# Kernel tuning notes

Measured on AMD Instinct MI355X. Metric: run time of the kernel, lower is better.

## Reference

```python
import jax, jax.numpy as jnp
import numpy as np
import math

B, CK, CV, H, W = 16, 64, 512, 56, 56


def setup_inputs() -> dict:
    key = jax.random.key(0)
    k1, k2, k3, k4 = jax.random.split(key, 4)
    return {
        "mk": jax.random.normal(k1, (B, CK, H, W), dtype=jnp.float32),
        "qk": jax.random.normal(k2, (B, CK, H, W), dtype=jnp.float32),
        "mv": jax.random.normal(k3, (B, CV, H, W), dtype=jnp.float32),
        "qv": jax.random.normal(k4, (B, CV, H, W), dtype=jnp.float32),
    }


def reference(mk, qk, mv, qv):
    b, ck, h, w = qk.shape
    cv = mv.shape[1]
    n = h * w
    qk_f = qk.reshape(b, ck, n)          # [B, CK, HW] query keys
    mk_f = mk.reshape(b, ck, -1)         # [B, CK, N_mem]
    # squared-L2 affinity (query-norm term is constant per column -> dropped, cancels in softmax)
    a = jnp.sum(mk_f * mk_f, axis=1)[:, :, None]                # [B, N_mem, 1]
    bb = 2.0 * jnp.einsum('bcn,bcm->bnm', mk_f, qk_f)           # [B, N_mem, HW]
    affinity = (-a + bb) / math.sqrt(ck)
    affinity = jax.nn.softmax(affinity, axis=1)                 # softmax over memory dim
    # readout: weighted sum of memory values
    mem = jnp.einsum('bcn,bnm->bcm', mv.reshape(b, cv, -1), affinity)
    mem = mem.reshape(b, cv, h, w)
    return mem, qv
```

## Files before the change

### kernel.cpp

```cpp
#include <hip/hip_runtime.h>


#define B_   16
#define CK_  64
#define CV_  512
#define N_   3136
#define NPAD 3200
#define TM   128
#define TN   128
#define NITER 25
#define NBLK32 100
#define NBLK16 200

typedef __bf16 bf16_t;
typedef bf16_t bf16x8 __attribute__((ext_vector_type(8)));
typedef bf16_t bf16x4 __attribute__((ext_vector_type(4)));
typedef float  f32x16 __attribute__((ext_vector_type(16)));
typedef float  f32x4  __attribute__((ext_vector_type(4)));

#define SCALE_DOT 0.36067376022224085f

__global__ __launch_bounds__(256) void prep_kq(const float* __restrict__ mk,
                                               const float* __restrict__ qk,
                                               bf16_t* __restrict__ Kf,
                                               bf16_t* __restrict__ Qf,
                                               float* __restrict__ a2) {
  int idx = blockIdx.x * 256 + threadIdx.x;
  int b = idx / NPAD, n = idx % NPAD;
  bool valid = n < N_;
  int l32n = n & 31, nblk = n >> 5;
  float ss = 0.f;
  const float* mkp = mk + (size_t)b * CK_ * N_ + n;
  const float* qkp = qk + (size_t)b * CK_ * N_ + n;
  bf16x8* Kf8 = (bf16x8*)Kf;
  bf16x8* Qf8 = (bf16x8*)Qf;
  #pragma unroll
  for (int cc = 0; cc < 8; cc++) {
    bf16x8 kv, qv8;
    #pragma unroll
    for (int j = 0; j < 8; j++) {
      int c = 8 * cc + j;
      float kx = valid ? mkp[(size_t)c * N_] : 0.f;
      float qx = valid ? qkp[(size_t)c * N_] : 0.f;
      ss += kx * kx;
      kv[j] = (bf16_t)kx;
      qv8[j] = (bf16_t)qx;
    }
    int s = cc >> 1, hh = cc & 1;
    size_t pos = (((size_t)b * NBLK32 + nblk) * 4 + s) * 64 + l32n + 32 * hh;
    Kf8[pos] = kv;
    Qf8[pos] = qv8;
  }
  a2[idx] = valid ? ss * 0.5f : 3.0e38f;
}

#define VCHUNK 512
__global__ __launch_bounds__(256) void prep_v(const float* __restrict__ mv,
                                              bf16_t* __restrict__ Vf) {
  __shared__ __align__(16) bf16_t T[32][VCHUNK];
  int wg = blockIdx.x;
  int chunk = wg % 7;
  int t2 = wg / 7;
  int cblk = t2 & 15;
  int b = t2 >> 4;
  int n0 = chunk * VCHUNK;
  int tid = threadIdx.x;

  const float* base = mv + ((size_t)b * CV_ + cblk * 32) * N_;
  #pragma unroll
  for (int rep = 0; rep < 16; rep++) {
    int idx = rep * 256 + tid;
    int cl = idx >> 7;
    int np = (idx & 127) * 4;
    int n = n0 + np;
    bf16x4 o;
    if (n < N_) {
      f32x4 v = *(const f32x4*)(base + (size_t)cl * N_ + n);
      #pragma unroll
      for (int j = 0; j < 4; j++) o[j] = (bf16_t)v[j];
    } else {
      #pragma unroll
      for (int j = 0; j < 4; j++) o[j] = (bf16_t)0.f;
    }
    *(bf16x4*)((char*)T + cl * (VCHUNK * 2) + ((np * 2) ^ ((cl & 7) << 4))) = o;
  }
  __syncthreads();

  bf16x8* Vf8 = (bf16x8*)Vf;
  size_t outbase = (((size_t)b * 16 + cblk) * NBLK16 + (n0 >> 4)) * 64;
  #pragma unroll
  for (int pass = 0; pass < 8; pass++) {
    int idx = pass * 256 + tid;
    int nb = idx >> 6;
    int ln = idx & 63;
    if (n0 + nb * 16 < NPAD) {
      int cl = ln & 31;
      int n_loc = nb * 16 + (ln >> 5) * 8;
      bf16x8 o = *(bf16x8*)((char*)T + cl * (VCHUNK * 2) +
                            ((n_loc * 2) ^ ((cl & 7) << 4)));
      Vf8[outbase + (size_t)nb * 64 + ln] = o;
    }
  }
}

__global__ __launch_bounds__(512, 2) void attn_main(const bf16_t* __restrict__ Kf,
                                                    const bf16_t* __restrict__ Qf,
                                                    const float* __restrict__ A2S,
                                                    const bf16_t* __restrict__ Vf,
                                                    const float* __restrict__ qv,
                                                    float* __restrict__ out) {
  const int xcd = blockIdx.x & 7;
  const int idx = blockIdx.x >> 3;
  const int q25 = idx / 25;
  const int b   = xcd * 2 + q25;
  const int m0  = (idx - q25 * 25) * TM;

  const int tid  = threadIdx.x;
  const int w    = tid >> 6;
  const int lane = tid & 63;
  const int l32  = lane & 31;
  const int h    = lane >> 5;
  const int g    = w >> 2;
  const int i    = w & 3;

  __shared__ __align__(16) char pool[65536];

  const bf16x8* Qf8 = (const bf16x8*)Qf;
  bf16x8 qfrag[2][4];
  #pragma unroll
  for (int jj = 0; jj < 2; jj++)
    #pragma unroll
    for (int s = 0; s < 4; s++)
      qfrag[jj][s] = Qf8[(((size_t)b * NBLK32 + (m0 >> 5) + 2 * g + jj) * 4 + s) * 64 + lane];

  f32x16 acc[2][4];
  #pragma unroll
  for (int cb = 0; cb < 2; cb++)
    #pragma unroll
    for (int mb = 0; mb < 4; mb++)
      #pragma unroll
      for (int r = 0; r < 16; r++) acc[cb][mb][r] = 0.f;

  float Lp[2] = {0.f, 0.f};
  const float*  a2b = A2S + (size_t)b * NPAD;
  const bf16x8* Kf8 = (const bf16x8*)Kf;
  const bf16x8* Vf8 = (const bf16x8*)Vf + (((size_t)b * 16 + 2 * w) * NBLK16) * 64 + lane;

  const int rswz = (l32 & 15) << 4;

  const f32x4* qsrc = (const f32x4*)qv;
  f32x4* qdst = (f32x4*)(out + (size_t)B_ * CV_ * N_);
  const size_t QT = (size_t)B_ * CV_ * N_ / 4;
  const size_t qbase = (size_t)blockIdx.x * 16384;
  f32x4 qr0, qr1;

  for (int iter = 0; iter < NITER; iter++) {
    const int n0 = iter * TN + 32 * i;

    if (iter >= 1 && iter <= 16) {
      size_t qi = qbase + (size_t)(iter - 1) * 1024 + tid;
      if (qi < QT) qdst[qi] = qr0;
      if (qi + 512 < QT) qdst[qi + 512] = qr1;
    }

    const bf16x8* kp = Kf8 + (((size_t)b * NBLK32 + (iter * 4 + i)) * 4) * 64 + lane;
    bf16x8 kf0 = kp[0], kf1 = kp[64], kf2 = kp[128], kf3 = kp[192];
    f32x4 na[4];
    #pragma unroll
    for (int t = 0; t < 4; t++)
      na[t] = *(const f32x4*)(a2b + n0 + 8 * t + 4 * h);
    const bf16x8* vp = Vf8 + (size_t)iter * 8 * 64;
    bf16x8 vfA[8];
    #pragma unroll
    for (int t = 0; t < 4; t++) {
      vfA[2 * t]     = vp[t * 64];
      vfA[2 * t + 1] = vp[t * 64 + NBLK16 * 64];
    }
    if (iter < 16) {
      size_t qi = qbase + (size_t)iter * 1024 + tid;
      if (qi < QT) qr0 = qsrc[qi];
      if (qi + 512 < QT) qr1 = qsrc[qi + 512];
    }

    char* Pb = pool + (iter & 1) * 32768;
    #pragma unroll
    for (int jj = 0; jj < 2; jj++) {
      f32x16 sacc;
      #pragma unroll
      for (int t = 0; t < 4; t++)
        #pragma unroll
        for (int q = 0; q < 4; q++) sacc[4 * t + q] = -na[t][q];
      sacc = __builtin_amdgcn_mfma_f32_32x32x16_bf16(kf0, qfrag[jj][0], sacc, 0, 0, 0);
      sacc = __builtin_amdgcn_mfma_f32_32x32x16_bf16(kf1, qfrag[jj][1], sacc, 0, 0, 0);
      sacc = __builtin_amdgcn_mfma_f32_32x32x16_bf16(kf2, qfrag[jj][2], sacc, 0, 0, 0);
      sacc = __builtin_amdgcn_mfma_f32_32x32x16_bf16(kf3, qfrag[jj][3], sacc, 0, 0, 0);

      const int wrow = 32 * (2 * g + jj) + l32;
      const int wswz = (l32 & 15) << 4;
      #pragma unroll
      for (int t = 0; t < 4; t++) {
        bf16x4 pk;
        #pragma unroll
        for (int q = 0; q < 4; q++) {
          float p = __builtin_amdgcn_exp2f(sacc[4 * t + q] * SCALE_DOT);
          Lp[jj] += p;
          pk[q] = (bf16_t)p;
        }
        int colb = 64 * i + 16 * t + 8 * h;
        *(bf16x4*)(Pb + wrow * 256 + (colb ^ wswz)) = pk;
      }
    }

    asm volatile("s_waitcnt lgkmcnt(0)" ::: "memory");
    __builtin_amdgcn_s_barrier();

    bf16x8 vfB[8];
    #pragma unroll
    for (int t = 0; t < 4; t++) {
      vfB[2 * t]     = vp[(t + 4) * 64];
      vfB[2 * t + 1] = vp[(t + 4) * 64 + NBLK16 * 64];
    }

    #pragma unroll
    for (int t = 0; t < 8; t++) {
      bf16x8 va0 = (t < 4) ? vfA[2 * t]     : vfB[2 * (t - 4)];
      bf16x8 va1 = (t < 4) ? vfA[2 * t + 1] : vfB[2 * (t - 4) + 1];
      #pragma unroll
      for (int mb = 0; mb < 4; mb++) {
        bf16x8 pf = *(const bf16x8*)(Pb + (32 * mb + l32) * 256 + ((32 * t + 16 * h) ^ rswz));
        acc[0][mb] = __builtin_amdgcn_mfma_f32_32x32x16_bf16(va0, pf, acc[0][mb], 0, 0, 0);
        acc[1][mb] = __builtin_amdgcn_mfma_f32_32x32x16_bf16(va1, pf, acc[1][mb], 0, 0, 0);
      }
    }
  }

  __syncthreads();
  Lp[0] += __shfl_xor(Lp[0], 32, 64);
  Lp[1] += __shfl_xor(Lp[1], 32, 64);
  float* Llds = (float*)pool;
  float* Linv = (float*)(pool + 2048);
  if (h == 0) {
    Llds[(w * 2 + 0) * 32 + l32] = Lp[0];
    Llds[(w * 2 + 1) * 32 + l32] = Lp[1];
  }
  __syncthreads();
  if (tid < 128) {
    int mb = tid >> 5, l = tid & 31;
    int g2 = mb >> 1, jj = mb & 1;
    float s = 0.f;
    #pragma unroll
    for (int ww = 0; ww < 4; ww++) s += Llds[((4 * g2 + ww) * 2 + jj) * 32 + l];
    Linv[tid] = 1.0f / s;
  }
  __syncthreads();

  #pragma unroll
  for (int cb = 0; cb < 2; cb++) {
    #pragma unroll
    for (int mb = 0; mb < 4; mb++) {
      int m = m0 + 32 * mb + l32;
      if (m < N_) {
        float rl = Linv[32 * mb + l32];
        #pragma unroll
        for (int reg = 0; reg < 16; reg++) {
          int r = (reg & 3) + 8 * (reg >> 2) + 4 * h;
          int c = 64 * w + 32 * cb + r;
          out[((size_t)b * CV_ + c) * N_ + m] = acc[cb][mb][reg] * rl;
        }
      }
    }
  }
}

extern "C" void kernel_launch(void* const* d_in, const int* in_sizes, int n_in,
                              void* d_out, int out_size, void* d_ws, size_t ws_size,
                              hipStream_t stream) {
  const float* mk = (const float*)d_in[0];
  const float* qk = (const float*)d_in[1];
  const float* mv = (const float*)d_in[2];
  const float* qv = (const float*)d_in[3];
  float* out = (float*)d_out;

  char* ws = (char*)d_ws;
  bf16_t* Kf = (bf16_t*)(ws);
  bf16_t* Qf = (bf16_t*)(ws + 6553600);
  float*  a2 = (float*)(ws + 13107200);
  bf16_t* Vf = (bf16_t*)(ws + 13312000);

  prep_kq<<<dim3((B_ * NPAD) / 256), dim3(256), 0, stream>>>(mk, qk, Kf, Qf, a2);
  prep_v<<<dim3(B_ * 16 * 7), dim3(256), 0, stream>>>(mv, Vf);
  attn_main<<<dim3(B_ * 25), dim3(512), 0, stream>>>(Kf, Qf, a2, Vf, qv, out);
}
```

Baseline: 725.6 us.

## Merge prep kernels and interleave QK MFMAs with qv copy in-iteration

The two preprocessing kernels become one launch, with block-index ranges split between the K/Q conversion and the V transpose. This removes one kernel boundary and lets both workloads run concurrently. In the main loop, the two score MFMA chains are interleaved across the key steps, with a sched_barrier added, to expose independent MFMA work. The qv passthrough copy now loads and stores within the same iteration instead of carrying registers across iterations, which may add load-latency stalls.

New measurement: 686.2 us. 5.4% less time.

```diff
diff --git a/kernel.cpp b/kernel.cpp
--- a/kernel.cpp
+++ b/kernel.cpp
@@ -19,86 +19,89 @@
 typedef float  f32x4  __attribute__((ext_vector_type(4)));
 
 #define SCALE_DOT 0.36067376022224085f
-
-__global__ __launch_bounds__(256) void prep_kq(const float* __restrict__ mk,
-                                               const float* __restrict__ qk,
-                                               bf16_t* __restrict__ Kf,
-                                               bf16_t* __restrict__ Qf,
-                                               float* __restrict__ a2) {
-  int idx = blockIdx.x * 256 + threadIdx.x;
-  int b = idx / NPAD, n = idx % NPAD;
-  bool valid = n < N_;
-  int l32n = n & 31, nblk = n >> 5;
-  float ss = 0.f;
-  const float* mkp = mk + (size_t)b * CK_ * N_ + n;
-  const float* qkp = qk + (size_t)b * CK_ * N_ + n;
-  bf16x8* Kf8 = (bf16x8*)Kf;
-  bf16x8* Qf8 = (bf16x8*)Qf;
-  #pragma unroll
-  for (int cc = 0; cc < 8; cc++) {
-    bf16x8 kv, qv8;
-    #pragma unroll
-    for (int j = 0; j < 8; j++) {
-      int c = 8 * cc + j;
-      float kx = valid ? mkp[(size_t)c * N_] : 0.f;
-      float qx = valid ? qkp[(size_t)c * N_] : 0.f;
-      ss += kx * kx;
-      kv[j] = (bf16_t)kx;
-      qv8[j] = (bf16_t)qx;
-    }
-    int s = cc >> 1, hh = cc & 1;
-    size_t pos = (((size_t)b * NBLK32 + nblk) * 4 + s) * 64 + l32n + 32 * hh;
-    Kf8[pos] = kv;
-    Qf8[pos] = qv8;
-  }
-  a2[idx] = valid ? ss * 0.5f : 3.0e38f;
-}
-
 #define VCHUNK 512
-__global__ __launch_bounds__(256) void prep_v(const float* __restrict__ mv,
-                                              bf16_t* __restrict__ Vf) {
+
+__global__ __launch_bounds__(256) void prep_all(const float* __restrict__ mk,
+                                                const float* __restrict__ qk,
+                                                const float* __restrict__ mv,
+                                                bf16_t* __restrict__ Kf,
+                                                bf16_t* __restrict__ Qf,
+                                                float* __restrict__ a2,
+                                                bf16_t* __restrict__ Vf) {
   __shared__ __align__(16) bf16_t T[32][VCHUNK];
   int wg = blockIdx.x;
-  int chunk = wg % 7;
-  int t2 = wg / 7;
-  int cblk = t2 & 15;
-  int b = t2 >> 4;
-  int n0 = chunk * VCHUNK;
   int tid = threadIdx.x;
 
-  const float* base = mv + ((size_t)b * CV_ + cblk * 32) * N_;
-  #pragma unroll
-  for (int rep = 0; rep < 16; rep++) {
-    int idx = rep * 256 + tid;
-    int cl = idx >> 7;
-    int np = (idx & 127) * 4;
-    int n = n0 + np;
-    bf16x4 o;
-    if (n < N_) {
-      f32x4 v = *(const f32x4*)(base + (size_t)cl * N_ + n);
-      #pragma unroll
-      for (int j = 0; j < 4; j++) o[j] = (bf16_t)v[j];
-    } else {
-      #pragma unroll
-      for (int j = 0; j < 4; j++) o[j] = (bf16_t)0.f;
-    }
-    *(bf16x4*)((char*)T + cl * (VCHUNK * 2) + ((np * 2) ^ ((cl & 7) << 4))) = o;
-  }
-  __syncthreads();
-
-  bf16x8* Vf8 = (bf16x8*)Vf;
-  size_t outbase = (((size_t)b * 16 + cblk) * NBLK16 + (n0 >> 4)) * 64;
-  #pragma unroll
-  for (int pass = 0; pass < 8; pass++) {
-    int idx = pass * 256 + tid;
-    int nb = idx >> 6;
-    int ln = idx & 63;
-    if (n0 + nb * 16 < NPAD) {
-      int cl = ln & 31;
-      int n_loc = nb * 16 + (ln >> 5) * 8;
-      bf16x8 o = *(bf16x8*)((char*)T + cl * (VCHUNK * 2) +
-                            ((n_loc * 2) ^ ((cl & 7) << 4)));
-      Vf8[outbase + (size_t)nb * 64 + ln] = o;
+  if (wg < 200) {
+    int idx = wg * 256 + tid;
+    int b = idx / NPAD, n = idx % NPAD;
+    bool valid = n < N_;
+    int l32n = n & 31, nblk = n >> 5;
+    float ss = 0.f;
+    const float* mkp = mk + (size_t)b * CK_ * N_ + n;
+    const float* qkp = qk + (size_t)b * CK_ * N_ + n;
+    bf16x8* Kf8 = (bf16x8*)Kf;
+    bf16x8* Qf8 = (bf16x8*)Qf;
+    #pragma unroll
+    for (int cc = 0; cc < 8; cc++) {
+      bf16x8 kv, qv8;
+      #pragma unroll
+      for (int j = 0; j < 8; j++) {
+        int c = 8 * cc + j;
+        float kx = valid ? mkp[(size_t)c * N_] : 0.f;
+        float qx = valid ? qkp[(size_t)c * N_] : 0.f;
+        ss += kx * kx;
+        kv[j] = (bf16_t)kx;
+        qv8[j] = (bf16_t)qx;
+      }
+      int s = cc >> 1, hh = cc & 1;
+      size_t pos = (((size_t)b * NBLK32 + nblk) * 4 + s) * 64 + l32n + 32 * hh;
+      Kf8[pos] = kv;
+      Qf8[pos] = qv8;
+    }
+    a2[idx] = valid ? ss * 0.5f : 3.0e38f;
+  } else {
+    int wg2 = wg - 200;
+    int chunk = wg2 % 7;
+    int t2 = wg2 / 7;
+    int cblk = t2 & 15;
+    int b = t2 >> 4;
+    int n0 = chunk * VCHUNK;
+
+    const float* base = mv + ((size_t)b * CV_ + cblk * 32) * N_;
+    #pragma unroll
+    for (int rep = 0; rep < 16; rep++) {
+      int idx = rep * 256 + tid;
+      int cl = idx >> 7;
+      int np = (idx & 127) * 4;
+      int n = n0 + np;
+      bf16x4 o;
+      if (n < N_) {
+        f32x4 v = *(const f32x4*)(base + (size_t)cl * N_ + n);
+        #pragma unroll
+        for (int j = 0; j < 4; j++) o[j] = (bf16_t)v[j];
+      } else {
+        #pragma unroll
+        for (int j = 0; j < 4; j++) o[j] = (bf16_t)0.f;
+      }
+      *(bf16x4*)((char*)T + cl * (VCHUNK * 2) + ((np * 2) ^ ((cl & 7) << 4))) = o;
+    }
+    __syncthreads();
+
+    bf16x8* Vf8 = (bf16x8*)Vf;
+    size_t outbase = (((size_t)b * 16 + cblk) * NBLK16 + (n0 >> 4)) * 64;
+    #pragma unroll
+    for (int pass = 0; pass < 8; pass++) {
+      int idx = pass * 256 + tid;
+      int nb = idx >> 6;
+      int ln = idx & 63;
+      if (n0 + nb * 16 < NPAD) {
+        int cl = ln & 31;
+        int n_loc = nb * 16 + (ln >> 5) * 8;
+        bf16x8 o = *(bf16x8*)((char*)T + cl * (VCHUNK * 2) +
+                              ((n_loc * 2) ^ ((cl & 7) << 4)));
+        Vf8[outbase + (size_t)nb * 64 + ln] = o;
+      }
     }
   }
 }
@@ -152,23 +155,39 @@
   f32x4* qdst = (f32x4*)(out + (size_t)B_ * CV_ * N_);
   const size_t QT = (size_t)B_ * CV_ * N_ / 4;
   const size_t qbase = (size_t)blockIdx.x * 16384;
-  f32x4 qr0, qr1;
 
   for (int iter = 0; iter < NITER; iter++) {
     const int n0 = iter * TN + 32 * i;
 
-    if (iter >= 1 && iter <= 16) {
-      size_t qi = qbase + (size_t)(iter - 1) * 1024 + tid;
-      if (qi < QT) qdst[qi] = qr0;
-      if (qi + 512 < QT) qdst[qi + 512] = qr1;
-    }
-
     const bf16x8* kp = Kf8 + (((size_t)b * NBLK32 + (iter * 4 + i)) * 4) * 64 + lane;
-    bf16x8 kf0 = kp[0], kf1 = kp[64], kf2 = kp[128], kf3 = kp[192];
+    bf16x8 kfr[4];
+    kfr[0] = kp[0]; kfr[1] = kp[64]; kfr[2] = kp[128]; kfr[3] = kp[192];
     f32x4 na[4];
     #pragma unroll
     for (int t = 0; t < 4; t++)
       na[t] = *(const f32x4*)(a2b + n0 + 8 * t + 4 * h);
+    f32x4 qr0, qr1;
+    const bool qval = iter < 16;
+    const size_t qi = qbase + (size_t)iter * 1024 + tid;
+    if (qval) {
+      if (qi < QT) qr0 = qsrc[qi];
+      if (qi + 512 < QT) qr1 = qsrc[qi + 512];
+    }
+
+    f32x16 sc[2];
+    #pragma unroll
+    for (int jj = 0; jj < 2; jj++)
+      #pragma unroll
+      for (int t = 0; t < 4; t++)
+        #pragma unroll
+        for (int q = 0; q < 4; q++) sc[jj][4 * t + q] = -na[t][q];
+    #pragma unroll
+    for (int s = 0; s < 4; s++) {
+      sc[0] = __builtin_amdgcn_mfma_f32_32x32x16_bf16(kfr[s], qfrag[0][s], sc[0], 0, 0, 0);
+      sc[1] = __builtin_amdgcn_mfma_f32_32x32x16_bf16(kfr[s], qfrag[1][s], sc[1], 0, 0, 0);
+    }
+    __builtin_amdgcn_sched_barrier(0);
+
     const bf16x8* vp = Vf8 + (size_t)iter * 8 * 64;
     bf16x8 vfA[8];
     #pragma unroll
@@ -176,25 +195,10 @@
       vfA[2 * t]     = vp[t * 64];
       vfA[2 * t + 1] = vp[t * 64 + NBLK16 * 64];
     }
-    if (iter < 16) {
-      size_t qi = qbase + (size_t)iter * 1024 + tid;
-      if (qi < QT) qr0 = qsrc[qi];
-      if (qi + 512 < QT) qr1 = qsrc[qi + 512];
-    }
 
     char* Pb = pool + (iter & 1) * 32768;
     #pragma unroll
     for (int jj = 0; jj < 2; jj++) {
-      f32x16 sacc;
-      #pragma unroll
-      for (int t = 0; t < 4; t++)
-        #pragma unroll
-        for (int q = 0; q < 4; q++) sacc[4 * t + q] = -na[t][q];
-      sacc = __builtin_amdgcn_mfma_f32_32x32x16_bf16(kf0, qfrag[jj][0], sacc, 0, 0, 0);
-      sacc = __builtin_amdgcn_mfma_f32_32x32x16_bf16(kf1, qfrag[jj][1], sacc, 0, 0, 0);
-      sacc = __builtin_amdgcn_mfma_f32_32x32x16_bf16(kf2, qfrag[jj][2], sacc, 0, 0, 0);
-      sacc = __builtin_amdgcn_mfma_f32_32x32x16_bf16(kf3, qfrag[jj][3], sacc, 0, 0, 0);
-
       const int wrow = 32 * (2 * g + jj) + l32;
       const int wswz = (l32 & 15) << 4;
       #pragma unroll
@@ -202,13 +206,18 @@
         bf16x4 pk;
         #pragma unroll
         for (int q = 0; q < 4; q++) {
-          float p = __builtin_amdgcn_exp2f(sacc[4 * t + q] * SCALE_DOT);
+          float p = __builtin_amdgcn_exp2f(sc[jj][4 * t + q] * SCALE_DOT);
           Lp[jj] += p;
           pk[q] = (bf16_t)p;
         }
         int colb = 64 * i + 16 * t + 8 * h;
         *(bf16x4*)(Pb + wrow * 256 + (colb ^ wswz)) = pk;
       }
+    }
+
+    if (qval) {
+      if (qi < QT) qdst[qi] = qr0;
+      if (qi + 512 < QT) qdst[qi + 512] = qr1;
     }
 
     asm volatile("s_waitcnt lgkmcnt(0)" ::: "memory");
@@ -287,7 +296,6 @@
   float*  a2 = (float*)(ws + 13107200);
   bf16_t* Vf = (bf16_t*)(ws + 13312000);
 
-  prep_kq<<<dim3((B_ * NPAD) / 256), dim3(256), 0, stream>>>(mk, qk, Kf, Qf, a2);
-  prep_v<<<dim3(B_ * 16 * 7), dim3(256), 0, stream>>>(mv, Vf);
+  prep_all<<<dim3(200 + B_ * 16 * 7), dim3(256), 0, stream>>>(mk, qk, mv, Kf, Qf, a2, Vf);
   attn_main<<<dim3(B_ * 25), dim3(512), 0, stream>>>(Kf, Qf, a2, Vf, qv, out);
 }
```
